# Optimization experiments

Measured on AMD Instinct MI355X. Metric: run time of the kernel, lower is better.

The kernel has to match this reference:

```python
import jax, jax.numpy as jnp
import numpy as np

T = 1024          # num tokens
H = 2048          # hidden_size
NH = 16           # attention heads
NKV = 4           # kv heads (GQA)
HD = 128          # head_dim
E = 32            # num routed experts
K = 4             # top_k
I = 1024          # moe_intermediate_size
NS = 1            # num_shared_experts
EPS = 1e-6
THETA = 600000.0  # rope base
SCALE = HD ** -0.5


def rmsnorm(x, w):
    return x * jax.lax.rsqrt(jnp.mean(x * x, axis=-1, keepdims=True) + EPS) * w


def rope(x, positions):
    # x: [T, n_heads, HD], neox-style rotation on full head_dim
    half = HD // 2
    inv_freq = 1.0 / (THETA ** (jnp.arange(half, dtype=jnp.float32) / half))
    ang = positions.astype(jnp.float32)[:, None] * inv_freq        # [T, half]
    cos = jnp.cos(ang)[:, None, :]
    sin = jnp.sin(ang)[:, None, :]
    x1, x2 = x[..., :half], x[..., half:]
    return jnp.concatenate([x1 * cos - x2 * sin, x1 * sin + x2 * cos], axis=-1)


def setup_inputs() -> dict:
    key = jax.random.key(0)
    ks = jax.random.split(key, 10)
    s = 0.02
    return {
        "hidden_states": jax.random.normal(ks[0], (T, H), dtype=jnp.float32),
        "positions": jnp.arange(T, dtype=jnp.int32),
        "w_rms1": jnp.ones((H,), jnp.float32),
        "w_rms2": jnp.ones((H,), jnp.float32),
        "w_qkv": jax.random.normal(ks[1], ((NH + 2 * NKV) * HD, H), jnp.float32) * s,
        "w_o": jax.random.normal(ks[2], (H, NH * HD), jnp.float32) * s,
        "w_router": jax.random.normal(ks[3], (E, H), jnp.float32) * s,
        "w1": jax.random.normal(ks[4], (E, H, I), jnp.float32) * s,   # expert gate proj
        "w3": jax.random.normal(ks[5], (E, H, I), jnp.float32) * s,   # expert up proj
        "w2": jax.random.normal(ks[6], (E, I, H), jnp.float32) * s,   # expert down proj
        "ws_gate_up": jax.random.normal(ks[7], (2 * I * NS, H), jnp.float32) * s,
        "ws_down": jax.random.normal(ks[8], (H, I * NS), jnp.float32) * s,
    }


def reference(hidden_states, positions, w_rms1, w_rms2, w_qkv, w_o, w_router,
              w1, w3, w2, ws_gate_up, ws_down):
    x = hidden_states
    # ---- attention block ----
    h = rmsnorm(x, w_rms1)
    qkv = h @ w_qkv.T                                   # [T, (NH+2NKV)*HD]
    q = qkv[:, : NH * HD].reshape(T, NH, HD)
    k = qkv[:, NH * HD : (NH + NKV) * HD].reshape(T, NKV, HD)
    v = qkv[:, (NH + NKV) * HD :].reshape(T, NKV, HD)
    q = rope(q, positions)
    k = rope(k, positions)
    rep = NH // NKV
    k = jnp.repeat(k, rep, axis=1)                      # [T, NH, HD]
    v = jnp.repeat(v, rep, axis=1)
    scores = jnp.einsum("thd,shd->hts", q, k) * SCALE   # [NH, T, T]
    causal = jnp.tril(jnp.ones((T, T), dtype=bool))
    scores = jnp.where(causal, scores, -jnp.inf)
    attn = jax.nn.softmax(scores, axis=-1)
    o = jnp.einsum("hts,shd->thd", attn, v).reshape(T, NH * HD)
    x = x + o @ w_o.T                                   # residual
    # ---- MoE block ----
    h2 = rmsnorm(x, w_rms2)
    # router in fp32 (router_dtype default)
    logits = h2.astype(jnp.float32) @ w_router.T        # [T, E]
    probs = jax.nn.softmax(logits, axis=-1)
    topv, topi = jax.lax.top_k(probs, K)                # [T, K]
    topv = topv / jnp.sum(topv, axis=-1, keepdims=True)  # norm_topk_prob
    combine = jnp.zeros((T, E), jnp.float32).at[jnp.arange(T)[:, None], topi].add(topv)
    combine = combine.astype(h2.dtype)                  # routed_scaling_factor = 1.0
    g = jnp.einsum("th,ehi->tei", h2, w1)               # [T, E, I]
    u = jnp.einsum("th,ehi->tei", h2, w3)
    a = jax.nn.silu(g) * u                              # SiluAndMul
    d = jnp.einsum("tei,eih->teh", a, w2)               # [T, E, H]
    routed = jnp.einsum("teh,te->th", d, combine)
    # shared expert MLP
    gu = h2 @ ws_gate_up.T                              # [T, 2*I*NS]
    gs, us = gu[:, : I * NS], gu[:, I * NS :]
    shared = (jax.nn.silu(gs) * us) @ ws_down.T
    return x + routed + shared
```

## Files before the change

### kernel.cpp

```cpp
#include <hip/hip_runtime.h>
#include <hip/hip_bf16.h>
#include <math.h>
#include <stdint.h>

#define T_ 1024
#define H_ 2048
#define NH_ 16
#define NKV_ 4
#define HD_ 128
#define E_ 32
#define TOPK_ 4
#define I_ 1024
#define QKVN_ 3072
#define EPS_ 1e-6f
#define THETA_ 600000.0f
#define SCALE_ 0.08838834764831845f

typedef unsigned short u16;
typedef u16 u16x4 __attribute__((ext_vector_type(4)));
typedef u16 u16x8 __attribute__((ext_vector_type(8)));
typedef __bf16 bf16x8 __attribute__((ext_vector_type(8)));
typedef float f32x4 __attribute__((ext_vector_type(4)));

__device__ __forceinline__ u16 f2b(float f) {
  unsigned u = __builtin_bit_cast(unsigned, f);
  u += 0x7FFFu + ((u >> 16) & 1u);
  return (u16)(u >> 16);
}
__device__ __forceinline__ float b2f(u16 x) {
  unsigned u = ((unsigned)x) << 16;
  return __builtin_bit_cast(float, u);
}
__device__ __forceinline__ int s2(int i) { return (i ^ (i >> 2)) & 3; }

__device__ __forceinline__ void gload16(const void* g, void* l) {
  __builtin_amdgcn_global_load_lds(
      reinterpret_cast<const __attribute__((address_space(1))) unsigned int*>(
          reinterpret_cast<uintptr_t>(g)),
      reinterpret_cast<__attribute__((address_space(3))) unsigned int*>(
          reinterpret_cast<uintptr_t>(l)),
      16, 0, 0);
}

template<int EPI, bool GATHER>
__global__ __launch_bounds__(512, 8) void moe_gemm_k(
    const u16* __restrict__ A, const float* __restrict__ B, const float* __restrict__ B2,
    float* __restrict__ O1, float* __restrict__ O2,
    int NW, int lda, int ldb, int K, int nx,
    const int* __restrict__ eoff, const int* __restrict__ tpre,
    const int* __restrict__ slots, const float* __restrict__ slotw,
    long long sBz, int* __restrict__ ctr)
{
  __shared__ u16 As[2][64 * 32];
  __shared__ u16 Bs[2][128 * 32];
  __shared__ int sh_idx;

  const int tid = threadIdx.x;
  const int lane = tid & 63;
  const int wv = tid >> 6;
  const int wm = wv >> 2, wn = wv & 3;
  const int kg = lane >> 4;
  const int cr = lane & 15;

  const int total = tpre[E_] * nx;

  for (;;) {
    if (tid == 0) sh_idx = atomicAdd(ctr, 1);
    __syncthreads();
    const int idx = sh_idx;
    __syncthreads();
    if (idx >= total) return;

    const int t = idx / nx;
    const int xx = idx - t * nx;
    int lo = 0, hi = E_;
    while (hi - lo > 1) { int mid = (lo + hi) >> 1; if (tpre[mid] <= t) lo = mid; else hi = mid; }
    const int e = lo;
    const int mb = t - tpre[e];
    const int goff = eoff[e];
    const int Mloc = eoff[e + 1] - goff;
    const int m0 = mb * 64;

    const float* Bp;
    float* Op;
    int n0;
    if constexpr (EPI == 0) {
      int wsel = xx >> 3;
      n0 = (xx & 7) * 128;
      Bp = (wsel ? B2 : B) + (long long)e * sBz;
      Op = wsel ? O2 : O1;
    } else {
      n0 = xx * 128;
      Bp = B + (long long)e * sBz;
      Op = O1;
    }
    const u16* Ae = GATHER ? A : (A + (long long)goff * lda);

    const u16* Abase = nullptr;
    if (wv < 4) {
      int r = wv * 16 + (lane >> 2);
      int rr = m0 + r;
      if (rr > Mloc - 1) rr = Mloc - 1;
      long long grow = GATHER ? (long long)slots[goff + rr] : (long long)rr;
      Abase = Ae + grow * (long long)lda + (((lane & 3) ^ s2(r)) << 3);
    }

    const int bn = tid & 127;
    const int bkc = tid >> 7;
    const float* Bbase = Bp + (long long)(bkc << 3) * ldb + n0 + bn;
    const int bws = bn * 32 + ((bkc ^ s2(bn)) << 3);

    float br[8];
    auto loadB = [&](int k0) {
      const float* p = Bbase + (long long)k0 * ldb;
      #pragma unroll
      for (int j = 0; j < 8; ++j) br[j] = p[(long long)j * ldb];
    };
    auto writeB = [&](int bf) {
      u16x8 o;
      #pragma unroll
      for (int j = 0; j < 8; ++j) o[j] = f2b(br[j]);
      *(u16x8*)(&Bs[bf][bws]) = o;
    };
    auto stageA = [&](int bf, int k0) {
      if (wv < 4) gload16(Abase + k0, &As[bf][wv * 512]);
    };

    f32x4 acc[2][2];
    #pragma unroll
    for (int m = 0; m < 2; ++m)
      #pragma unroll
      for (int n = 0; n < 2; ++n)
        acc[m][n] = f32x4{0.f, 0.f, 0.f, 0.f};

    int aoff[2], boff[2];
    #pragma unroll
    for (int m = 0; m < 2; ++m) {
      int r = wm * 32 + m * 16 + cr;
      aoff[m] = r * 32 + ((kg ^ s2(r)) << 3);
    }
    #pragma unroll
    for (int n = 0; n < 2; ++n) {
      int c = wn * 32 + n * 16 + cr;
      boff[n] = c * 32 + ((kg ^ s2(c)) << 3);
    }

    loadB(0);
    stageA(0, 0);
    writeB(0);
    __syncthreads();

    int buf = 0;
    for (int ks = 0; ks < K; ks += 32) {
      bool more = (ks + 32) < K;
      if (more) { loadB(ks + 32); stageA(buf ^ 1, ks + 32); }
      const u16* Ap = &As[buf][0];
      const u16* Bq = &Bs[buf][0];
      bf16x8 af[2], bfr[2];
      #pragma unroll
      for (int m = 0; m < 2; ++m)
        af[m] = __builtin_bit_cast(bf16x8, *(const u16x8*)(Ap + aoff[m]));
      #pragma unroll
      for (int n = 0; n < 2; ++n)
        bfr[n] = __builtin_bit_cast(bf16x8, *(const u16x8*)(Bq + boff[n]));
      #pragma unroll
      for (int m = 0; m < 2; ++m)
        #pragma unroll
        for (int n = 0; n < 2; ++n)
          acc[m][n] = __builtin_amdgcn_mfma_f32_16x16x32_bf16(af[m], bfr[n], acc[m][n], 0, 0, 0);
      if (more) writeB(buf ^ 1);
      __syncthreads();
      buf ^= 1;
    }

    const int rq = lane >> 4;
    #pragma unroll
    for (int m = 0; m < 2; ++m) {
      #pragma unroll
      for (int j = 0; j < 4; ++j) {
        int row = m0 + wm * 32 + m * 16 + rq * 4 + j;
        if (row >= Mloc) continue;
        if constexpr (EPI == 0) {
          float* dst = Op + (long long)(goff + row) * NW;
          #pragma unroll
          for (int n = 0; n < 2; ++n) {
            int col = n0 + wn * 32 + n * 16 + cr;
            dst[col] = acc[m][n][j];
          }
        } else {
          int tok = slots[goff + row];
          float wgt = slotw[goff + row];
          float* dst = Op + (long long)tok * NW;
          #pragma unroll
          for (int n = 0; n < 2; ++n) {
            int col = n0 + wn * 32 + n * 16 + cr;
            atomicAdd(dst + col, wgt * acc[m][n][j]);
          }
        }
      }
    }
  }
}

template<typename TB, int EPI, int CAUSAL>
__global__ __launch_bounds__(512, 8) void dense_gemm_k(
    const u16* __restrict__ A, const TB* __restrict__ B,
    u16* __restrict__ Cb, float* __restrict__ Cf,
    const float* __restrict__ res1, const float* __restrict__ res2,
    int K, int lda, int ldb, int ldc, float alpha,
    long long sAz, long long sBz, long long sCz, int bdivz)
{
  __shared__ u16 As[2][64 * 32];
  __shared__ u16 Bs[2][128 * 32];

  const int m0 = blockIdx.y * 64;
  const int n0 = blockIdx.x * 128;
  if (CAUSAL == 1 && n0 > m0 + 63) return;
  const long long z = blockIdx.z;
  const u16* Ae = A + z * sAz;
  const TB* Be = B + (long long)(z / bdivz) * sBz;
  u16* Cwb = Cb ? Cb + z * sCz : nullptr;

  int kend = K;
  if (CAUSAL == 2) { int ke = m0 + 64; if (ke < kend) kend = ke; }

  const int tid = threadIdx.x;
  const int lane = tid & 63;
  const int wv = tid >> 6;
  const int wm = wv >> 2, wn = wv & 3;

  const u16* Abase = nullptr;
  if (wv < 4) {
    int r = wv * 16 + (lane >> 2);
    Abase = Ae + (long long)(m0 + r) * lda + (((lane & 3) ^ s2(r)) << 3);
  }
  auto stageA = [&](int bf, int k0) {
    if (wv < 4) gload16(Abase + k0, &As[bf][wv * 512]);
  };

  const u16* Bu16base = nullptr;
  const float* Bf32base = nullptr;
  int bws = 0;
  if constexpr (sizeof(TB) == 2) {
    int r = wv * 16 + (lane >> 2);
    Bu16base = (const u16*)Be + (long long)(n0 + r) * ldb + (((lane & 3) ^ s2(r)) << 3);
  } else {
    int bn = tid >> 2, bkq = tid & 3;
    Bf32base = (const float*)Be + (long long)(n0 + bn) * ldb + (bkq << 3);
    bws = bn * 32 + ((bkq ^ s2(bn)) << 3);
  }
  float br[8];
  auto loadB = [&](int k0) {
    const float* p = Bf32base + k0;
    float4 a = *(const float4*)p;
    float4 b = *(const float4*)(p + 4);
    br[0] = a.x; br[1] = a.y; br[2] = a.z; br[3] = a.w;
    br[4] = b.x; br[5] = b.y; br[6] = b.z; br[7] = b.w;
  };
  auto writeB = [&](int bf) {
    u16x8 o;
    #pragma unroll
    for (int j = 0; j < 8; ++j) o[j] = f2b(br[j]);
    *(u16x8*)(&Bs[bf][bws]) = o;
  };
  auto stageBu = [&](int bf, int k0) {
    gload16(Bu16base + k0, &Bs[bf][wv * 512]);
  };

  f32x4 acc[2][2];
  #pragma unroll
  for (int m = 0; m < 2; ++m)
    #pragma unroll
    for (int n = 0; n < 2; ++n)
      acc[m][n] = f32x4{0.f, 0.f, 0.f, 0.f};

  const int kg = lane >> 4;
  const int cr = lane & 15;

  int aoff[2], boff[2];
  #pragma unroll
  for (int m = 0; m < 2; ++m) {
    int r = wm * 32 + m * 16 + cr;
    aoff[m] = r * 32 + ((kg ^ s2(r)) << 3);
  }
  #pragma unroll
  for (int n = 0; n < 2; ++n) {
    int c = wn * 32 + n * 16 + cr;
    boff[n] = c * 32 + ((kg ^ s2(c)) << 3);
  }

  if constexpr (sizeof(TB) == 4) {
    loadB(0); stageA(0, 0); writeB(0);
  } else {
    stageA(0, 0); stageBu(0, 0);
  }
  __syncthreads();

  int buf = 0;
  for (int ks = 0; ks < kend; ks += 32) {
    bool more = (ks + 32) < kend;
    if (more) {
      if constexpr (sizeof(TB) == 4) { loadB(ks + 32); stageA(buf ^ 1, ks + 32); }
      else { stageA(buf ^ 1, ks + 32); stageBu(buf ^ 1, ks + 32); }
    }
    const u16* Ap = &As[buf][0];
    const u16* Bq = &Bs[buf][0];
    bf16x8 af[2], bfr[2];
    #pragma unroll
    for (int m = 0; m < 2; ++m)
      af[m] = __builtin_bit_cast(bf16x8, *(const u16x8*)(Ap + aoff[m]));
    #pragma unroll
    for (int n = 0; n < 2; ++n)
      bfr[n] = __builtin_bit_cast(bf16x8, *(const u16x8*)(Bq + boff[n]));
    #pragma unroll
    for (int m = 0; m < 2; ++m)
      #pragma unroll
      for (int n = 0; n < 2; ++n)
        acc[m][n] = __builtin_amdgcn_mfma_f32_16x16x32_bf16(af[m], bfr[n], acc[m][n], 0, 0, 0);
    if constexpr (sizeof(TB) == 4) { if (more) writeB(buf ^ 1); }
    __syncthreads();
    buf ^= 1;
  }

  const int rq = lane >> 4;
  #pragma unroll
  for (int m = 0; m < 2; ++m) {
    #pragma unroll
    for (int j = 0; j < 4; ++j) {
      int row = m0 + wm * 32 + m * 16 + rq * 4 + j;
      #pragma unroll
      for (int n = 0; n < 2; ++n) {
        int col = n0 + wn * 32 + n * 16 + cr;
        float v = acc[m][n][j];
        long long o = (long long)row * ldc + col;
        if constexpr (EPI == 0) {
          Cwb[o] = f2b(v);
        } else if constexpr (EPI == 1) {
          Cwb[o] = f2b(v * alpha);
        } else if constexpr (EPI == 2) {
          Cf[o] = res1[o] + v;
        } else {
          Cf[o] = res1[o] + res2[o] + v;
        }
      }
    }
  }
}

__global__ __launch_bounds__(256) void vtrans_k(const u16* __restrict__ v_r,
                                                u16* __restrict__ v_t) {
  __shared__ u16 t[64][72];
  int kv = blockIdx.z;
  int s0 = blockIdx.x * 64, d0 = blockIdx.y * 64;
  int tid = threadIdx.x;
  int sr = tid >> 2, dq = (tid & 3) * 16;
  const u16* src = v_r + ((long long)kv * T_ + s0 + sr) * HD_ + d0 + dq;
  *(u16x8*)&t[sr][dq] = *(const u16x8*)src;
  *(u16x8*)&t[sr][dq + 8] = *(const u16x8*)(src + 8);
  __syncthreads();
  int dr = tid >> 2, sq = (tid & 3) * 16;
  u16* dst = v_t + ((long long)kv * HD_ + d0 + dr) * T_ + s0 + sq;
  u16x8 o0, o1;
  #pragma unroll
  for (int j = 0; j < 8; ++j) { o0[j] = t[sq + j][dr]; o1[j] = t[sq + 8 + j][dr]; }
  *(u16x8*)dst = o0;
  *(u16x8*)(dst + 8) = o1;
}

__global__ __launch_bounds__(256) void rmsnorm_k(const float* __restrict__ x,
                                                 const float* __restrict__ w,
                                                 u16* __restrict__ outb,
                                                 float* __restrict__ outf) {
  int t = blockIdx.x;
  int tid = threadIdx.x;
  const float* xr = x + (long long)t * H_;
  float4 a = *(const float4*)(xr + tid * 8);
  float4 b = *(const float4*)(xr + tid * 8 + 4);
  float ss = a.x * a.x + a.y * a.y + a.z * a.z + a.w * a.w +
             b.x * b.x + b.y * b.y + b.z * b.z + b.w * b.w;
  #pragma unroll
  for (int o = 32; o; o >>= 1) ss += __shfl_down(ss, o);
  __shared__ float red[4];
  if ((tid & 63) == 0) red[tid >> 6] = ss;
  __syncthreads();
  float sc = rsqrtf((red[0] + red[1] + red[2] + red[3]) * (1.0f / H_) + EPS_);
  float vo[8] = {a.x, a.y, a.z, a.w, b.x, b.y, b.z, b.w};
  const float* wr = w + tid * 8;
  u16x8 ob;
  #pragma unroll
  for (int q = 0; q < 8; ++q) {
    float val = vo[q] * sc * wr[q];
    ob[q] = f2b(val);
    if (outf) outf[(long long)t * H_ + tid * 8 + q] = val;
  }
  *(u16x8*)(outb + (long long)t * H_ + tid * 8) = ob;
}

__global__ __launch_bounds__(256) void rope_k(const u16* __restrict__ qkv,
                                              const int* __restrict__ pos,
                                              u16* __restrict__ q_r,
                                              u16* __restrict__ k_r,
                                              u16* __restrict__ v_r) {
  int t = blockIdx.x;
  int tid = threadIdx.x;
  float p = (float)pos[t];
  const u16* row = qkv + (long long)t * QKVN_;
  const float cfac = logf(THETA_) * (1.0f / 64.0f);
  #pragma unroll
  for (int it = 0; it < 4; ++it) {
    int item = it * 256 + tid;
    int h = item >> 6, d = item & 63;
    float inv = expf(-cfac * (float)d);
    float ang = p * inv;
    float c = cosf(ang), s = sinf(ang);
    float x1v = b2f(row[h * 128 + d]);
    float x2v = b2f(row[h * 128 + 64 + d]);
    u16* dst = q_r + ((long long)h * T_ + t) * HD_;
    dst[d] = f2b(x1v * c - x2v * s);
    dst[d + 64] = f2b(x1v * s + x2v * c);
  }
  {
    int item = tid;
    int kv = item >> 6, d = item & 63;
    float inv = expf(-cfac * (float)d);
    float ang = p * inv;
    float c = cosf(ang), s = sinf(ang);
    float x1v = b2f(row[NH_ * HD_ + kv * 128 + d]);
    float x2v = b2f(row[NH_ * HD_ + kv * 128 + 64 + d]);
    u16* dst = k_r + ((long long)kv * T_ + t) * HD_;
    dst[d] = f2b(x1v * c - x2v * s);
    dst[d + 64] = f2b(x1v * s + x2v * c);
  }
  #pragma unroll
  for (int it = 0; it < 2; ++it) {
    int item = it * 256 + tid;
    int kv = item >> 7, d = item & 127;
    v_r[((long long)kv * T_ + t) * HD_ + d] = row[(NH_ + NKV_) * HD_ + kv * 128 + d];
  }
}

__global__ __launch_bounds__(64) void softmax_k(u16* __restrict__ P) {
  int r = blockIdx.x;
  int h = r >> 10, i = r & 1023;
  u16* row = P + ((long long)h * T_ + i) * T_;
  int lane = threadIdx.x;
  int n = i + 1;
  float vals[16];
  float mx = -1e30f;
  #pragma unroll
  for (int it = 0; it < 16; ++it) {
    int j = it * 64 + lane;
    float s = (j < n) ? b2f(row[j]) : -1e30f;
    vals[it] = s;
    mx = fmaxf(mx, s);
  }
  #pragma unroll
  for (int o = 32; o; o >>= 1) mx = fmaxf(mx, __shfl_xor(mx, o));
  float sum = 0.f;
  #pragma unroll
  for (int it = 0; it < 16; ++it) {
    int j = it * 64 + lane;
    float e = (j < n) ? __expf(vals[it] - mx) : 0.f;
    vals[it] = e;
    sum += e;
  }
  #pragma unroll
  for (int o = 32; o; o >>= 1) sum += __shfl_xor(sum, o);
  float inv = 1.f / sum;
  #pragma unroll
  for (int it = 0; it < 16; ++it) {
    int j = it * 64 + lane;
    row[j] = f2b(vals[it] * inv);
  }
}

__global__ __launch_bounds__(64) void router_k(const float* __restrict__ h2,
                                               const float* __restrict__ wr,
                                               float* __restrict__ logits) {
  int b = blockIdx.x;
  int t = b >> 5, e = b & 31;
  const float* xr = h2 + (long long)t * H_;
  const float* wv = wr + (long long)e * H_;
  int lane = threadIdx.x;
  float s = 0.f;
  #pragma unroll
  for (int it = 0; it < 8; ++it) {
    int h = it * 256 + lane * 4;
    float4 a = *(const float4*)(xr + h);
    float4 w4 = *(const float4*)(wv + h);
    s += a.x * w4.x + a.y * w4.y + a.z * w4.z + a.w * w4.w;
  }
  #pragma unroll
  for (int o = 32; o; o >>= 1) s += __shfl_xor(s, o);
  if (lane == 0) logits[b] = s;
}

__global__ __launch_bounds__(256) void topk_k(const float* __restrict__ logits,
                                              int* __restrict__ topi,
                                              float* __restrict__ topw) {
  int t = blockIdx.x * 256 + threadIdx.x;
  if (t >= T_) return;
  float l[E_];
  #pragma unroll
  for (int e = 0; e < E_; ++e) l[e] = logits[t * E_ + e];
  int sel[TOPK_];
  float sv[TOPK_];
  unsigned used = 0;
  for (int j = 0; j < TOPK_; ++j) {
    float best = -1e30f;
    int bi = 0;
    for (int e = 0; e < E_; ++e) {
      if (used & (1u << e)) continue;
      if (l[e] > best) { best = l[e]; bi = e; }
    }
    used |= 1u << bi;
    sel[j] = bi;
    sv[j] = best;
  }
  float mx = sv[0];
  float s = 0.f;
  #pragma unroll
  for (int j = 0; j < TOPK_; ++j) { sv[j] = __expf(sv[j] - mx); s += sv[j]; }
  float inv = 1.f / s;
  #pragma unroll
  for (int j = 0; j < TOPK_; ++j) {
    topi[t * TOPK_ + j] = sel[j];
    topw[t * TOPK_ + j] = sv[j] * inv;
  }
}

__global__ __launch_bounds__(256) void hist_k(const int* __restrict__ topi, int* __restrict__ cnt) {
  int idx = blockIdx.x * 256 + threadIdx.x;
  if (idx < T_ * TOPK_) atomicAdd(&cnt[topi[idx]], 1);
}

__global__ __launch_bounds__(64) void scan_k(const int* __restrict__ cnt,
                                             int* __restrict__ eoff,
                                             int* __restrict__ cursor,
                                             int* __restrict__ tpre) {
  if (threadIdx.x == 0) {
    int s = 0, tt = 0;
    for (int e = 0; e < E_; ++e) {
      eoff[e] = s; cursor[e] = s; tpre[e] = tt;
      tt += (cnt[e] + 63) >> 6;
      s += cnt[e];
    }
    eoff[E_] = s; tpre[E_] = tt;
  }
}

__global__ __launch_bounds__(256) void scatter_k(const int* __restrict__ topi,
                                                 const float* __restrict__ topw,
                                                 int* __restrict__ cursor,
                                                 int* __restrict__ slots,
                                                 float* __restrict__ slotw) {
  int idx = blockIdx.x * 256 + threadIdx.x;
  if (idx >= T_ * TOPK_) return;
  int e = topi[idx];
  int pos = atomicAdd(&cursor[e], 1);
  slots[pos] = idx >> 2;
  slotw[pos] = topw[idx];
}

__global__ __launch_bounds__(256) void silumul_f_k(const float* __restrict__ g,
                                                   const float* __restrict__ u,
                                                   u16* __restrict__ a) {
  long long idx = ((long long)blockIdx.x * 256 + threadIdx.x) * 8;
  float4 g0 = *(const float4*)(g + idx);
  float4 g1 = *(const float4*)(g + idx + 4);
  float4 u0 = *(const float4*)(u + idx);
  float4 u1 = *(const float4*)(u + idx + 4);
  float gv[8] = {g0.x, g0.y, g0.z, g0.w, g1.x, g1.y, g1.z, g1.w};
  float uv[8] = {u0.x, u0.y, u0.z, u0.w, u1.x, u1.y, u1.z, u1.w};
  u16x8 o;
  #pragma unroll
  for (int q = 0; q < 8; ++q) {
    float x = gv[q];
    float sl = x / (1.f + __expf(-x));
    o[q] = f2b(sl * uv[q]);
  }
  *(u16x8*)(a + idx) = o;
}

__global__ __launch_bounds__(256) void sharedact_k(const u16* __restrict__ gu,
                                                   u16* __restrict__ act) {
  long long idx = ((long long)blockIdx.x * 256 + threadIdx.x) * 8;
  long long t = idx >> 10;
  int i = (int)(idx & 1023);
  const u16* row = gu + t * (2 * I_);
  u16x8 g = *(const u16x8*)(row + i);
  u16x8 u = *(const u16x8*)(row + I_ + i);
  u16x8 o;
  #pragma unroll
  for (int q = 0; q < 8; ++q) {
    float x = b2f(g[q]);
    float y = b2f(u[q]);
    float sl = x / (1.f + __expf(-x));
    o[q] = f2b(sl * y);
  }
  *(u16x8*)(act + t * I_ + i) = o;
}

extern "C" void kernel_launch(void* const* d_in, const int* in_sizes, int n_in,
                              void* d_out, int out_size, void* d_ws, size_t ws_size,
                              hipStream_t stream) {
  const float* x        = (const float*)d_in[0];
  const int* positions  = (const int*)d_in[1];
  const float* w_rms1   = (const float*)d_in[2];
  const float* w_rms2   = (const float*)d_in[3];
  const float* w_qkv    = (const float*)d_in[4];
  const float* w_o      = (const float*)d_in[5];
  const float* w_router = (const float*)d_in[6];
  const float* w1       = (const float*)d_in[7];
  const float* w3       = (const float*)d_in[8];
  const float* w2       = (const float*)d_in[9];
  const float* ws_gu    = (const float*)d_in[10];
  const float* ws_dn    = (const float*)d_in[11];
  float* out = (float*)d_out;

  char* ws = (char*)d_ws;
  size_t off = 0;
  auto alloc = [&](size_t bytes) {
    size_t o = off;
    off = (off + bytes + 255) & ~(size_t)255;
    return (void*)(ws + o);
  };
  u16*  h1b     = (u16*)alloc((size_t)T_ * H_ * 2);
  u16*  qkvb    = (u16*)alloc((size_t)T_ * QKVN_ * 2);
  u16*  q_r     = (u16*)alloc((size_t)NH_ * T_ * HD_ * 2);
  u16*  k_r     = (u16*)alloc((size_t)NKV_ * T_ * HD_ * 2);
  u16*  v_r     = (u16*)alloc((size_t)NKV_ * T_ * HD_ * 2);
  u16*  v_t     = (u16*)alloc((size_t)NKV_ * HD_ * T_ * 2);
  u16*  scoresP = (u16*)alloc((size_t)NH_ * T_ * T_ * 2);
  u16*  o_attn  = (u16*)alloc((size_t)T_ * H_ * 2);
  float* x1     = (float*)alloc((size_t)T_ * H_ * 4);
  float* h2f    = (float*)alloc((size_t)T_ * H_ * 4);
  u16*  h2b     = (u16*)alloc((size_t)T_ * H_ * 2);
  u16*  gub     = (u16*)alloc((size_t)T_ * 2 * I_ * 2);
  u16*  actsh   = (u16*)alloc((size_t)T_ * I_ * 2);
  float* logits = (float*)alloc((size_t)T_ * E_ * 4);
  int*  topi    = (int*)alloc((size_t)T_ * TOPK_ * 4);
  float* topw   = (float*)alloc((size_t)T_ * TOPK_ * 4);
  int*  cnt     = (int*)alloc(E_ * 4);
  int*  eoffp   = (int*)alloc((E_ + 1) * 4);
  int*  cursor  = (int*)alloc(E_ * 4);
  int*  tpre    = (int*)alloc((E_ + 1) * 4);
  int*  wqctr   = (int*)alloc(2 * 4);
  int*  slots   = (int*)alloc((size_t)T_ * TOPK_ * 4);
  float* slotw  = (float*)alloc((size_t)T_ * TOPK_ * 4);
  u16*  a_g     = (u16*)alloc((size_t)T_ * TOPK_ * I_ * 2);
  float* routed = (float*)alloc((size_t)T_ * H_ * 4);

  float* g_f32 = (float*)scoresP;
  float* u_f32 = g_f32 + (size_t)T_ * TOPK_ * I_;

  hipMemsetAsync(routed, 0, (size_t)T_ * H_ * 4, stream);
  hipMemsetAsync(cnt, 0, E_ * 4, stream);
  hipMemsetAsync(wqctr, 0, 2 * 4, stream);

  rmsnorm_k<<<T_, 256, 0, stream>>>(x, w_rms1, h1b, nullptr);

  dense_gemm_k<float, 0, 0><<<dim3(24, 16, 1), 512, 0, stream>>>(
      h1b, w_qkv, qkvb, nullptr, nullptr, nullptr,
      H_, H_, H_, QKVN_, 1.f, 0, 0, 0, 1);

  rope_k<<<T_, 256, 0, stream>>>(qkvb, positions, q_r, k_r, v_r);
  vtrans_k<<<dim3(16, 2, 4), 256, 0, stream>>>(v_r, v_t);

  dense_gemm_k<u16, 1, 1><<<dim3(8, 16, NH_), 512, 0, stream>>>(
      q_r, k_r, scoresP, nullptr, nullptr, nullptr,
      HD_, HD_, HD_, T_, SCALE_,
      (long long)T_ * HD_, (long long)T_ * HD_, (long long)T_ * T_, NH_ / NKV_);

  softmax_k<<<NH_ * T_, 64, 0, stream>>>(scoresP);

  dense_gemm_k<u16, 0, 2><<<dim3(1, 16, NH_), 512, 0, stream>>>(
      scoresP, v_t, o_attn, nullptr, nullptr, nullptr,
      T_, T_, T_, H_, 1.f,
      (long long)T_ * T_, (long long)HD_ * T_, (long long)HD_, NH_ / NKV_);

  dense_gemm_k<float, 2, 0><<<dim3(16, 16, 1), 512, 0, stream>>>(
      o_attn, w_o, nullptr, x1, x, nullptr,
      H_, H_, H_, H_, 1.f, 0, 0, 0, 1);

  rmsnorm_k<<<T_, 256, 0, stream>>>(x1, w_rms2, h2b, h2f);

  router_k<<<T_ * E_, 64, 0, stream>>>(h2f, w_router, logits);
  topk_k<<<4, 256, 0, stream>>>(logits, topi, topw);
  hist_k<<<16, 256, 0, stream>>>(topi, cnt);
  scan_k<<<1, 64, 0, stream>>>(cnt, eoffp, cursor, tpre);
  scatter_k<<<16, 256, 0, stream>>>(topi, topw, cursor, slots, slotw);

  moe_gemm_k<0, true><<<1024, 512, 0, stream>>>(
      h2b, w1, w3, g_f32, u_f32,
      I_, H_, I_, H_, 16, eoffp, tpre, slots, nullptr,
      (long long)H_ * I_, wqctr);
  silumul_f_k<<<(T_ * TOPK_ * I_) / (256 * 8), 256, 0, stream>>>(g_f32, u_f32, a_g);

  moe_gemm_k<1, false><<<1024, 512, 0, stream>>>(
      a_g, w2, nullptr, routed, nullptr,
      H_, I_, H_, I_, 16, eoffp, tpre, slots, slotw,
      (long long)I_ * H_, wqctr + 1);

  dense_gemm_k<float, 0, 0><<<dim3(16, 16, 1), 512, 0, stream>>>(
      h2b, ws_gu, gub, nullptr, nullptr, nullptr,
      H_, H_, H_, 2 * I_, 1.f, 0, 0, 0, 1);
  sharedact_k<<<(T_ * I_) / (256 * 8), 256, 0, stream>>>(gub, actsh);

  dense_gemm_k<float, 4, 0><<<dim3(16, 16, 1), 512, 0, stream>>>(
      actsh, ws_dn, nullptr, out, x1, routed,
      I_, I_, I_, H_, 1.f, 0, 0, 0, 1);
}
```

Measured before the change: 668.3 us.

## Replace persistent atomic work queue in MoE GEMM with static grid; batch router per token

The MoE grouped GEMM drops its persistent-block loop, which pulled tiles from a global atomic counter, and instead maps each block statically to one (m-tile, n-tile) pair. The grid is sized to an upper bound of 1536 blocks, and blocks beyond the real tile count exit early. This removes the per-tile atomic and two barriers, plus the counter memset. The router kernel now runs one 256-thread block per token: it stages the hidden row in LDS and computes all 32 expert logits there, instead of launching one 64-thread block per (token, expert). The cost is empty blocks at launch and no dynamic load balancing.

```diff
diff --git a/kernel.cpp b/kernel.cpp
--- a/kernel.cpp
+++ b/kernel.cpp
@@ -46,14 +46,39 @@
 __global__ __launch_bounds__(512, 8) void moe_gemm_k(
     const u16* __restrict__ A, const float* __restrict__ B, const float* __restrict__ B2,
     float* __restrict__ O1, float* __restrict__ O2,
-    int NW, int lda, int ldb, int K, int nx,
+    int NW, int lda, int ldb, int K,
     const int* __restrict__ eoff, const int* __restrict__ tpre,
-    const int* __restrict__ slots, const float* __restrict__ slotw,
-    long long sBz, int* __restrict__ ctr)
+    const int* __restrict__ slots, const float* __restrict__ slotw, long long sBz)
 {
   __shared__ u16 As[2][64 * 32];
   __shared__ u16 Bs[2][128 * 32];
-  __shared__ int sh_idx;
+
+  const int idx = blockIdx.x;
+  const int t = idx >> 4;
+  const int xx = idx & 15;
+  if (t >= tpre[E_]) return;
+  int lo = 0, hi = E_;
+  while (hi - lo > 1) { int mid = (lo + hi) >> 1; if (tpre[mid] <= t) lo = mid; else hi = mid; }
+  const int e = lo;
+  const int mb = t - tpre[e];
+  const int goff = eoff[e];
+  const int Mloc = eoff[e + 1] - goff;
+  const int m0 = mb * 64;
+
+  const float* Bp;
+  float* Op;
+  int n0;
+  if constexpr (EPI == 0) {
+    int wsel = xx >> 3;
+    n0 = (xx & 7) * 128;
+    Bp = (wsel ? B2 : B) + (long long)e * sBz;
+    Op = wsel ? O2 : O1;
+  } else {
+    n0 = xx * 128;
+    Bp = B + (long long)e * sBz;
+    Op = O1;
+  }
+  const u16* Ae = GATHER ? A : (A + (long long)goff * lda);
 
   const int tid = threadIdx.x;
   const int lane = tid & 63;
@@ -62,140 +87,105 @@
   const int kg = lane >> 4;
   const int cr = lane & 15;
 
-  const int total = tpre[E_] * nx;
-
-  for (;;) {
-    if (tid == 0) sh_idx = atomicAdd(ctr, 1);
-    __syncthreads();
-    const int idx = sh_idx;
-    __syncthreads();
-    if (idx >= total) return;
-
-    const int t = idx / nx;
-    const int xx = idx - t * nx;
-    int lo = 0, hi = E_;
-    while (hi - lo > 1) { int mid = (lo + hi) >> 1; if (tpre[mid] <= t) lo = mid; else hi = mid; }
-    const int e = lo;
-    const int mb = t - tpre[e];
-    const int goff = eoff[e];
-    const int Mloc = eoff[e + 1] - goff;
-    const int m0 = mb * 64;
-
-    const float* Bp;
-    float* Op;
-    int n0;
-    if constexpr (EPI == 0) {
-      int wsel = xx >> 3;
-      n0 = (xx & 7) * 128;
-      Bp = (wsel ? B2 : B) + (long long)e * sBz;
-      Op = wsel ? O2 : O1;
-    } else {
-      n0 = xx * 128;
-      Bp = B + (long long)e * sBz;
-      Op = O1;
-    }
-    const u16* Ae = GATHER ? A : (A + (long long)goff * lda);
-
-    const u16* Abase = nullptr;
-    if (wv < 4) {
-      int r = wv * 16 + (lane >> 2);
-      int rr = m0 + r;
-      if (rr > Mloc - 1) rr = Mloc - 1;
-      long long grow = GATHER ? (long long)slots[goff + rr] : (long long)rr;
-      Abase = Ae + grow * (long long)lda + (((lane & 3) ^ s2(r)) << 3);
-    }
-
-    const int bn = tid & 127;
-    const int bkc = tid >> 7;
-    const float* Bbase = Bp + (long long)(bkc << 3) * ldb + n0 + bn;
-    const int bws = bn * 32 + ((bkc ^ s2(bn)) << 3);
-
-    float br[8];
-    auto loadB = [&](int k0) {
-      const float* p = Bbase + (long long)k0 * ldb;
-      #pragma unroll
-      for (int j = 0; j < 8; ++j) br[j] = p[(long long)j * ldb];
-    };
-    auto writeB = [&](int bf) {
-      u16x8 o;
-      #pragma unroll
-      for (int j = 0; j < 8; ++j) o[j] = f2b(br[j]);
-      *(u16x8*)(&Bs[bf][bws]) = o;
-    };
-    auto stageA = [&](int bf, int k0) {
-      if (wv < 4) gload16(Abase + k0, &As[bf][wv * 512]);
-    };
-
-    f32x4 acc[2][2];
+  const u16* Abase = nullptr;
+  if (wv < 4) {
+    int r = wv * 16 + (lane >> 2);
+    int rr = m0 + r;
+    if (rr > Mloc - 1) rr = Mloc - 1;
+    long long grow = GATHER ? (long long)slots[goff + rr] : (long long)rr;
+    Abase = Ae + grow * (long long)lda + (((lane & 3) ^ s2(r)) << 3);
+  }
+
+  const int bn = tid & 127;
+  const int bkc = tid >> 7;
+  const float* Bbase = Bp + (long long)(bkc << 3) * ldb + n0 + bn;
+  const int bws = bn * 32 + ((bkc ^ s2(bn)) << 3);
+
+  float br[8];
+  auto loadB = [&](int k0) {
+    const float* p = Bbase + (long long)k0 * ldb;
+    #pragma unroll
+    for (int j = 0; j < 8; ++j) br[j] = p[(long long)j * ldb];
+  };
+  auto writeB = [&](int bf) {
+    u16x8 o;
+    #pragma unroll
+    for (int j = 0; j < 8; ++j) o[j] = f2b(br[j]);
+    *(u16x8*)(&Bs[bf][bws]) = o;
+  };
+  auto stageA = [&](int bf, int k0) {
+    if (wv < 4) gload16(Abase + k0, &As[bf][wv * 512]);
+  };
+
+  f32x4 acc[2][2];
+  #pragma unroll
+  for (int m = 0; m < 2; ++m)
+    #pragma unroll
+    for (int n = 0; n < 2; ++n)
+      acc[m][n] = f32x4{0.f, 0.f, 0.f, 0.f};
+
+  int aoff[2], boff[2];
+  #pragma unroll
+  for (int m = 0; m < 2; ++m) {
+    int r = wm * 32 + m * 16 + cr;
+    aoff[m] = r * 32 + ((kg ^ s2(r)) << 3);
+  }
+  #pragma unroll
+  for (int n = 0; n < 2; ++n) {
+    int c = wn * 32 + n * 16 + cr;
+    boff[n] = c * 32 + ((kg ^ s2(c)) << 3);
+  }
+
+  loadB(0);
+  stageA(0, 0);
+  writeB(0);
+  __syncthreads();
+
+  int buf = 0;
+  for (int ks = 0; ks < K; ks += 32) {
+    bool more = (ks + 32) < K;
+    if (more) { loadB(ks + 32); stageA(buf ^ 1, ks + 32); }
+    const u16* Ap = &As[buf][0];
+    const u16* Bq = &Bs[buf][0];
+    bf16x8 af[2], bfr[2];
+    #pragma unroll
+    for (int m = 0; m < 2; ++m)
+      af[m] = __builtin_bit_cast(bf16x8, *(const u16x8*)(Ap + aoff[m]));
+    #pragma unroll
+    for (int n = 0; n < 2; ++n)
+      bfr[n] = __builtin_bit_cast(bf16x8, *(const u16x8*)(Bq + boff[n]));
     #pragma unroll
     for (int m = 0; m < 2; ++m)
       #pragma unroll
       for (int n = 0; n < 2; ++n)
-        acc[m][n] = f32x4{0.f, 0.f, 0.f, 0.f};
-
-    int aoff[2], boff[2];
-    #pragma unroll
-    for (int m = 0; m < 2; ++m) {
-      int r = wm * 32 + m * 16 + cr;
-      aoff[m] = r * 32 + ((kg ^ s2(r)) << 3);
-    }
-    #pragma unroll
-    for (int n = 0; n < 2; ++n) {
-      int c = wn * 32 + n * 16 + cr;
-      boff[n] = c * 32 + ((kg ^ s2(c)) << 3);
-    }
-
-    loadB(0);
-    stageA(0, 0);
-    writeB(0);
+        acc[m][n] = __builtin_amdgcn_mfma_f32_16x16x32_bf16(af[m], bfr[n], acc[m][n], 0, 0, 0);
+    if (more) writeB(buf ^ 1);
     __syncthreads();
-
-    int buf = 0;
-    for (int ks = 0; ks < K; ks += 32) {
-      bool more = (ks + 32) < K;
-      if (more) { loadB(ks + 32); stageA(buf ^ 1, ks + 32); }
-      const u16* Ap = &As[buf][0];
-      const u16* Bq = &Bs[buf][0];
-      bf16x8 af[2], bfr[2];
-      #pragma unroll
-      for (int m = 0; m < 2; ++m)
-        af[m] = __builtin_bit_cast(bf16x8, *(const u16x8*)(Ap + aoff[m]));
-      #pragma unroll
-      for (int n = 0; n < 2; ++n)
-        bfr[n] = __builtin_bit_cast(bf16x8, *(const u16x8*)(Bq + boff[n]));
-      #pragma unroll
-      for (int m = 0; m < 2; ++m)
+    buf ^= 1;
+  }
+
+  const int rq = lane >> 4;
+  #pragma unroll
+  for (int m = 0; m < 2; ++m) {
+    #pragma unroll
+    for (int j = 0; j < 4; ++j) {
+      int row = m0 + wm * 32 + m * 16 + rq * 4 + j;
+      if (row >= Mloc) continue;
+      if constexpr (EPI == 0) {
+        float* dst = Op + (long long)(goff + row) * NW;
         #pragma unroll
-        for (int n = 0; n < 2; ++n)
-          acc[m][n] = __builtin_amdgcn_mfma_f32_16x16x32_bf16(af[m], bfr[n], acc[m][n], 0, 0, 0);
-      if (more) writeB(buf ^ 1);
-      __syncthreads();
-      buf ^= 1;
-    }
-
-    const int rq = lane >> 4;
-    #pragma unroll
-    for (int m = 0; m < 2; ++m) {
-      #pragma unroll
-      for (int j = 0; j < 4; ++j) {
-        int row = m0 + wm * 32 + m * 16 + rq * 4 + j;
-        if (row >= Mloc) continue;
-        if constexpr (EPI == 0) {
-          float* dst = Op + (long long)(goff + row) * NW;
-          #pragma unroll
-          for (int n = 0; n < 2; ++n) {
-            int col = n0 + wn * 32 + n * 16 + cr;
-            dst[col] = acc[m][n][j];
-          }
-        } else {
-          int tok = slots[goff + row];
-          float wgt = slotw[goff + row];
-          float* dst = Op + (long long)tok * NW;
-          #pragma unroll
-          for (int n = 0; n < 2; ++n) {
-            int col = n0 + wn * 32 + n * 16 + cr;
-            atomicAdd(dst + col, wgt * acc[m][n][j]);
-          }
+        for (int n = 0; n < 2; ++n) {
+          int col = n0 + wn * 32 + n * 16 + cr;
+          dst[col] = acc[m][n][j];
+        }
+      } else {
+        int tok = slots[goff + row];
+        float wgt = slotw[goff + row];
+        float* dst = Op + (long long)tok * NW;
+        #pragma unroll
+        for (int n = 0; n < 2; ++n) {
+          int col = n0 + wn * 32 + n * 16 + cr;
+          atomicAdd(dst + col, wgt * acc[m][n][j]);
         }
       }
     }
@@ -474,25 +464,33 @@
   }
 }
 
-__global__ __launch_bounds__(64) void router_k(const float* __restrict__ h2,
-                                               const float* __restrict__ wr,
-                                               float* __restrict__ logits) {
-  int b = blockIdx.x;
-  int t = b >> 5, e = b & 31;
-  const float* xr = h2 + (long long)t * H_;
-  const float* wv = wr + (long long)e * H_;
-  int lane = threadIdx.x;
-  float s = 0.f;
-  #pragma unroll
-  for (int it = 0; it < 8; ++it) {
-    int h = it * 256 + lane * 4;
-    float4 a = *(const float4*)(xr + h);
-    float4 w4 = *(const float4*)(wv + h);
-    s += a.x * w4.x + a.y * w4.y + a.z * w4.z + a.w * w4.w;
-  }
-  #pragma unroll
-  for (int o = 32; o; o >>= 1) s += __shfl_xor(s, o);
-  if (lane == 0) logits[b] = s;
+__global__ __launch_bounds__(256) void router2_k(const float* __restrict__ h2,
+                                                 const float* __restrict__ wr,
+                                                 float* __restrict__ logits) {
+  __shared__ float hrow[H_];
+  int t = blockIdx.x;
+  int tid = threadIdx.x;
+  float4 a = *(const float4*)(h2 + (long long)t * H_ + tid * 8);
+  float4 b = *(const float4*)(h2 + (long long)t * H_ + tid * 8 + 4);
+  *(float4*)&hrow[tid * 8] = a;
+  *(float4*)&hrow[tid * 8 + 4] = b;
+  __syncthreads();
+  int wv = tid >> 6, lane = tid & 63;
+  #pragma unroll
+  for (int ei = 0; ei < 8; ++ei) {
+    int e = wv * 8 + ei;
+    const float* wrow = wr + (long long)e * H_;
+    float s = 0.f;
+    #pragma unroll
+    for (int it = 0; it < 8; ++it) {
+      int k = it * 256 + lane * 4;
+      float4 w4 = *(const float4*)(wrow + k);
+      s += hrow[k] * w4.x + hrow[k + 1] * w4.y + hrow[k + 2] * w4.z + hrow[k + 3] * w4.w;
+    }
+    #pragma unroll
+    for (int o = 32; o; o >>= 1) s += __shfl_xor(s, o);
+    if (lane == 0) logits[t * E_ + e] = s;
+  }
 }
 
 __global__ __launch_bounds__(256) void topk_k(const float* __restrict__ logits,
@@ -645,7 +643,6 @@
   int*  eoffp   = (int*)alloc((E_ + 1) * 4);
   int*  cursor  = (int*)alloc(E_ * 4);
   int*  tpre    = (int*)alloc((E_ + 1) * 4);
-  int*  wqctr   = (int*)alloc(2 * 4);
   int*  slots   = (int*)alloc((size_t)T_ * TOPK_ * 4);
   float* slotw  = (float*)alloc((size_t)T_ * TOPK_ * 4);
   u16*  a_g     = (u16*)alloc((size_t)T_ * TOPK_ * I_ * 2);
@@ -656,7 +653,6 @@
 
   hipMemsetAsync(routed, 0, (size_t)T_ * H_ * 4, stream);
   hipMemsetAsync(cnt, 0, E_ * 4, stream);
-  hipMemsetAsync(wqctr, 0, 2 * 4, stream);
 
   rmsnorm_k<<<T_, 256, 0, stream>>>(x, w_rms1, h1b, nullptr);
 
@@ -685,22 +681,20 @@
 
   rmsnorm_k<<<T_, 256, 0, stream>>>(x1, w_rms2, h2b, h2f);
 
-  router_k<<<T_ * E_, 64, 0, stream>>>(h2f, w_router, logits);
+  router2_k<<<T_, 256, 0, stream>>>(h2f, w_router, logits);
   topk_k<<<4, 256, 0, stream>>>(logits, topi, topw);
   hist_k<<<16, 256, 0, stream>>>(topi, cnt);
   scan_k<<<1, 64, 0, stream>>>(cnt, eoffp, cursor, tpre);
   scatter_k<<<16, 256, 0, stream>>>(topi, topw, cursor, slots, slotw);
 
-  moe_gemm_k<0, true><<<1024, 512, 0, stream>>>(
+  moe_gemm_k<0, true><<<1536, 512, 0, stream>>>(
       h2b, w1, w3, g_f32, u_f32,
-      I_, H_, I_, H_, 16, eoffp, tpre, slots, nullptr,
-      (long long)H_ * I_, wqctr);
+      I_, H_, I_, H_, eoffp, tpre, slots, nullptr, (long long)H_ * I_);
   silumul_f_k<<<(T_ * TOPK_ * I_) / (256 * 8), 256, 0, stream>>>(g_f32, u_f32, a_g);
 
-  moe_gemm_k<1, false><<<1024, 512, 0, stream>>>(
+  moe_gemm_k<1, false><<<1536, 512, 0, stream>>>(
       a_g, w2, nullptr, routed, nullptr,
-      H_, I_, H_, I_, 16, eoffp, tpre, slots, slotw,
-      (long long)I_ * H_, wqctr + 1);
+      H_, I_, H_, I_, eoffp, tpre, slots, slotw, (long long)I_ * H_);
 
   dense_gemm_k<float, 0, 0><<<dim3(16, 16, 1), 512, 0, stream>>>(
       h2b, ws_gu, gub, nullptr, nullptr, nullptr,
```

New measurement: 589.1 us. 11.9% less time.
